# Optimization experiments

Measured on AMD Instinct MI355X. Metric: run time of the kernel, lower is better.

## Reference

```python
import jax, jax.numpy as jnp
import numpy as np

N = 50000      # nodes (atoms)
E = 1000000    # edges (bonds within cutoff)
L = 3          # num_interactions
G = 512        # graphs in batch
H = 128        # hidden_channels == num_filters
NGAUSS = 50    # num_gaussians
CUTOFF = 10.0
ZMAX = 100     # atomic numbers, < num_embeddings=120
LOG2 = float(np.log(2.0))


def ssp(x):
    # ShiftedSoftplus: softplus(x) - log(2)
    return jax.nn.softplus(x) - LOG2


def setup_inputs() -> dict:
    key = jax.random.key(0)
    ks = jax.random.split(key, 16)

    def w(k, shape, fan_in):
        return jax.random.normal(k, shape, jnp.float32) / np.sqrt(fan_in)

    z = jax.random.randint(ks[0], (N,), 1, ZMAX)
    edge_src = jax.random.randint(ks[1], (E,), 0, N)
    edge_dst = jax.random.randint(ks[2], (E,), 0, N)
    batch = jnp.sort(jax.random.randint(ks[3], (N,), 0, G))
    edge_weight = jax.random.uniform(ks[4], (E,), jnp.float32) * CUTOFF  # distances in [0, cutoff)
    edge_attr = jax.random.normal(ks[5], (E, NGAUSS), jnp.float32)       # gaussian-smeared distances
    return {
        'z': z, 'edge_src': edge_src, 'edge_dst': edge_dst, 'batch': batch,
        'num_graphs': G,
        'edge_weight': edge_weight, 'edge_attr': edge_attr,
        'emb': w(ks[6], (120, H), 1.0),
        'mlp_w1': w(ks[7], (L, NGAUSS, H), NGAUSS), 'mlp_b1': jnp.zeros((L, H), jnp.float32),
        'mlp_w2': w(ks[8], (L, H, H), H), 'mlp_b2': jnp.zeros((L, H), jnp.float32),
        'cf_w1': w(ks[9], (L, H, H), H),
        'cf_w2': w(ks[10], (L, H, H), H), 'cf_b2': jnp.zeros((L, H), jnp.float32),
        'lin_w': w(ks[11], (L, H, H), H), 'lin_b': jnp.zeros((L, H), jnp.float32),
        'ro_w1': w(ks[12], (H, 5 * H), H), 'ro_b1': jnp.zeros((5 * H,), jnp.float32),
        'ro_w2': w(ks[13], (5 * H, H), 5 * H), 'ro_b2': jnp.zeros((H,), jnp.float32),
        'ro_w3': w(ks[14], (H, 1), H), 'ro_b3': jnp.zeros((1,), jnp.float32),
    }


def reference(z, edge_src, edge_dst, batch, num_graphs, edge_weight, edge_attr,
              emb, mlp_w1, mlp_b1, mlp_w2, mlp_b2, cf_w1, cf_w2, cf_b2,
              lin_w, lin_b, ro_w1, ro_b1, ro_w2, ro_b2, ro_w3, ro_b3):
    n_nodes = z.shape[0]
    # simple_z=True: h = relu(Embedding(z))
    h = jax.nn.relu(emb[z])                                   # [N, H]
    # cosine cutoff on distances (shared across blocks)
    C = 0.5 * (jnp.cos(edge_weight * jnp.pi / CUTOFF) + 1.0)  # [E]
    for l in range(L):
        # SchNet filter network on edge attributes
        Wf = ssp(edge_attr @ mlp_w1[l] + mlp_b1[l]) @ mlp_w2[l] + mlp_b2[l]
        Wf = Wf * C[:, None]                                  # [E, H]
        x = h @ cf_w1[l]                                      # CFConv.lin1 (no bias)
        msg = x[edge_src] * Wf                                # gather + filter modulation
        agg = jax.ops.segment_sum(msg, edge_dst, num_segments=n_nodes)  # scatter-add
        x = agg @ cf_w2[l] + cf_b2[l]                         # CFConv.lin2
        x = ssp(x) @ lin_w[l] + lin_b[l]                      # act + block linear
        h = h + x                                             # residual from model forward
    # ReadOutLayer
    hh = ssp(h @ ro_w1 + ro_b1)                               # [N, 5H]
    pooled = jax.ops.segment_sum(hh, batch, num_segments=num_graphs)  # segment_csr 'add'
    out = ssp(pooled @ ro_w2 + ro_b2) @ ro_w3 + ro_b3         # [G, 1]
    return out
```

## Files before the change

kernel.cpp:

```cpp
#include <hip/hip_runtime.h>
#include <math.h>

#define N_NODES 50000
#define N_EDGES 1000000
#define LAYERS  3
#define G_GRAPHS 512
#define H 128
#define NG 50
#define PI_F 3.14159265358979323846f
#define LOG2_F 0.6931471805599453f

typedef __attribute__((ext_vector_type(4))) float f32x4;
typedef __attribute__((ext_vector_type(8))) short short8;

__device__ __forceinline__ float ssp(float v) {
    float t = __expf(-fabsf(v));
    return fmaxf(v, 0.0f) + __logf(1.0f + t) - LOG2_F;
}

__device__ __forceinline__ unsigned short f2bf(float f) {
    unsigned u = __float_as_uint(f);
    unsigned r = (u + 0x7fff + ((u >> 16) & 1)) >> 16;
    return (unsigned short)r;
}
__device__ __forceinline__ float bf2f(unsigned short h) {
    return __uint_as_float((unsigned)h << 16);
}

__global__ __launch_bounds__(256) void init_h(const int* __restrict__ z,
                                              const float* __restrict__ emb,
                                              float* __restrict__ h) {
    int idx = blockIdx.x * 256 + threadIdx.x;
    if (idx >= N_NODES * (H / 4)) return;
    int n = idx >> 5;
    int c4 = idx & 31;
    int zv = z[n];
    float4 v = *(const float4*)(emb + (size_t)zv * H + c4 * 4);
    v.x = fmaxf(v.x, 0.f); v.y = fmaxf(v.y, 0.f);
    v.z = fmaxf(v.z, 0.f); v.w = fmaxf(v.w, 0.f);
    *(float4*)(h + (size_t)n * H + c4 * 4) = v;
}

__global__ __launch_bounds__(256) void hist_kernel(const int* __restrict__ edst,
                                                   int* __restrict__ cnt) {
    int e = blockIdx.x * 256 + threadIdx.x;
    if (e < N_EDGES) atomicAdd(&cnt[edst[e]], 1);
}

__global__ __launch_bounds__(1024) void scan_kernel(const int* __restrict__ cnt,
                                                    int* __restrict__ cur) {
    __shared__ int wsum[16];
    __shared__ int carry_s;
    int tid = threadIdx.x;
    int wid = tid >> 6, lane = tid & 63;
    if (tid == 0) carry_s = 0;
    __syncthreads();
    for (int base = 0; base < N_NODES; base += 1024) {
        int i = base + tid;
        int v = (i < N_NODES) ? cnt[i] : 0;
        int s = v;
#pragma unroll
        for (int d = 1; d < 64; d <<= 1) {
            int t = __shfl_up(s, d, 64);
            if (lane >= d) s += t;
        }
        if (lane == 63) wsum[wid] = s;
        __syncthreads();
        if (wid == 0) {
            int ws = (lane < 16) ? wsum[lane] : 0;
#pragma unroll
            for (int d = 1; d < 16; d <<= 1) {
                int t = __shfl_up(ws, d, 64);
                if (lane >= d) ws += t;
            }
            if (lane < 16) wsum[lane] = ws;
        }
        __syncthreads();
        int waveoff = (wid > 0) ? wsum[wid - 1] : 0;
        int carry = carry_s;
        if (i < N_NODES) cur[i] = carry + waveoff + s - v;
        __syncthreads();
        if (tid == 1023) carry_s = carry + wsum[15];
    }
}

__global__ __launch_bounds__(256) void scatter_kernel(const int* __restrict__ edst,
                                                      int* __restrict__ cur,
                                                      int* __restrict__ perm) {
    int e = blockIdx.x * 256 + threadIdx.x;
    if (e < N_EDGES) {
        int p = atomicAdd(&cur[edst[e]], 1);
        perm[p] = e;
    }
}

__global__ __launch_bounds__(256) void conv_w(const float* __restrict__ mlp_w1,
                                              const float* __restrict__ mlp_w2,
                                              unsigned short* __restrict__ w1t,
                                              unsigned short* __restrict__ w2t) {
    int idx = blockIdx.x * 256 + threadIdx.x;
    const int n1 = LAYERS * 128 * 64;
    if (idx < n1) {
        int l = idx / (128 * 64);
        int rem = idx - l * 128 * 64;
        int col = rem >> 6, k = rem & 63;
        float v = (k < NG) ? mlp_w1[(size_t)l * NG * H + (size_t)k * H + col] : 0.f;
        w1t[idx] = f2bf(v);
        return;
    }
    int idx2 = idx - n1;
    if (idx2 < LAYERS * 128 * 128) {
        int l = idx2 / (128 * 128);
        int rem = idx2 - l * 128 * 128;
        int col = rem >> 7, k = rem & 127;
        w2t[idx2] = f2bf(mlp_w2[(size_t)l * H * H + (size_t)k * H + col]);
    }
}

__global__ __launch_bounds__(256) void conv_nodew(const float* __restrict__ src,
                                                  unsigned short* __restrict__ hi,
                                                  unsigned short* __restrict__ lo,
                                                  int ncols) {
    int idx = blockIdx.x * 256 + threadIdx.x;
    if (idx >= ncols * 128) return;
    int col = idx >> 7, k = idx & 127;
    float v = src[(size_t)k * ncols + col];
    unsigned short h16 = f2bf(v);
    hi[idx] = h16;
    lo[idx] = f2bf(v - bf2f(h16));
}

#define F_BIAS 1
#define F_POOL 8

template <int FLAGS>
__global__ __launch_bounds__(256, 4) void node_gemm_mfma(const float* __restrict__ A,
                                                         const unsigned short* __restrict__ BtHi,
                                                         const unsigned short* __restrict__ BtLo,
                                                         const float* __restrict__ bias,
                                                         float* __restrict__ Out,
                                                         const int* __restrict__ batch,
                                                         int nRows, int NC) {
    __shared__ __align__(16) char ldsHi[64 * 256];
    __shared__ __align__(16) char ldsLo[64 * 256];
    int tid = threadIdx.x;
    int rowBase = blockIdx.x * 64;
    int colOff = blockIdx.y * 128;
    int rlim = nRows - rowBase; if (rlim > 64) rlim = 64;

    for (int idx = tid; idx < 64 * 32; idx += 256) {
        int r = idx >> 5, q = idx & 31;
        float4 v = make_float4(0.f, 0.f, 0.f, 0.f);
        if (r < rlim) v = *(const float4*)(A + (size_t)(rowBase + r) * H + q * 4);
        unsigned short h0 = f2bf(v.x), h1 = f2bf(v.y), h2 = f2bf(v.z), h3 = f2bf(v.w);
        unsigned short l0 = f2bf(v.x - bf2f(h0)), l1 = f2bf(v.y - bf2f(h1));
        unsigned short l2 = f2bf(v.z - bf2f(h2)), l3 = f2bf(v.w - bf2f(h3));
        int byte = (r << 8) + (q << 3);
        byte ^= (r & 7) << 4;
        *(uint2*)(ldsHi + byte) = make_uint2((unsigned)h0 | ((unsigned)h1 << 16),
                                             (unsigned)h2 | ((unsigned)h3 << 16));
        *(uint2*)(ldsLo + byte) = make_uint2((unsigned)l0 | ((unsigned)l1 << 16),
                                             (unsigned)l2 | ((unsigned)l3 << 16));
    }
    __syncthreads();

    int w = tid >> 6, lane = tid & 63;
    int lg = lane >> 4, cg = lane & 15;
    int swA = (cg & 7) << 4;

    f32x4 acc[4][2];
#pragma unroll
    for (int n = 0; n < 2; ++n) {
        float b = (FLAGS & F_BIAS) ? bias[colOff + w * 32 + n * 16 + cg] : 0.f;
        f32x4 t = {b, b, b, b};
#pragma unroll
        for (int m = 0; m < 4; ++m) acc[m][n] = t;
    }

#pragma unroll
    for (int kc = 0; kc < 4; ++kc) {
        short8 aHi[4], aLo[4], bHi[2], bLo[2];
#pragma unroll
        for (int m = 0; m < 4; ++m) {
            int byte = ((m * 16 + cg) << 8) + ((kc * 32 + lg * 8) << 1);
            aHi[m] = *(short8*)(ldsHi + (byte ^ swA));
            aLo[m] = *(short8*)(ldsLo + (byte ^ swA));
        }
#pragma unroll
        for (int n = 0; n < 2; ++n) {
            size_t off = (size_t)(colOff + w * 32 + n * 16 + cg) * 128 + kc * 32 + lg * 8;
            bHi[n] = *(const short8*)(BtHi + off);
            bLo[n] = *(const short8*)(BtLo + off);
        }
#pragma unroll
        for (int m = 0; m < 4; ++m)
#pragma unroll
            for (int n = 0; n < 2; ++n) {
                acc[m][n] = __builtin_amdgcn_mfma_f32_16x16x32_bf16(aHi[m], bHi[n], acc[m][n], 0, 0, 0);
                acc[m][n] = __builtin_amdgcn_mfma_f32_16x16x32_bf16(aLo[m], bHi[n], acc[m][n], 0, 0, 0);
                acc[m][n] = __builtin_amdgcn_mfma_f32_16x16x32_bf16(aHi[m], bLo[n], acc[m][n], 0, 0, 0);
            }
    }

    if (FLAGS & F_POOL) {
        int cur = -1;
        float s[2] = {0.f, 0.f};
#pragma unroll
        for (int m = 0; m < 4; ++m) {
#pragma unroll
            for (int i = 0; i < 4; ++i) {
                int row = m * 16 + lg * 4 + i;
                int b = (row < rlim) ? batch[rowBase + row] : -1;
                if (b != cur) {
                    if (cur >= 0) {
#pragma unroll
                        for (int n = 0; n < 2; ++n)
                            unsafeAtomicAdd(Out + (size_t)cur * NC + colOff + w * 32 + n * 16 + cg, s[n]);
                    }
                    cur = b;
                    s[0] = 0.f; s[1] = 0.f;
                }
                if (b >= 0) {
#pragma unroll
                    for (int n = 0; n < 2; ++n) s[n] += ssp(acc[m][n][i]);
                }
            }
        }
        if (cur >= 0) {
#pragma unroll
            for (int n = 0; n < 2; ++n)
                unsafeAtomicAdd(Out + (size_t)cur * NC + colOff + w * 32 + n * 16 + cg, s[n]);
        }
    } else {
#pragma unroll
        for (int m = 0; m < 4; ++m)
#pragma unroll
            for (int i = 0; i < 4; ++i) {
                int row = m * 16 + lg * 4 + i;
                if (row < rlim) {
#pragma unroll
                    for (int n = 0; n < 2; ++n)
                        Out[(size_t)(rowBase + row) * NC + colOff + w * 32 + n * 16 + cg] = acc[m][n][i];
                }
            }
    }
}

__global__ __launch_bounds__(256, 4) void node_gemm2_mfma(const float* __restrict__ Agg,
                                                          const unsigned short* __restrict__ W2hi,
                                                          const unsigned short* __restrict__ W2lo,
                                                          const float* __restrict__ b2,
                                                          const unsigned short* __restrict__ WLhi,
                                                          const unsigned short* __restrict__ WLlo,
                                                          const float* __restrict__ bl,
                                                          float* __restrict__ Hio,
                                                          int nRows) {
    __shared__ __align__(16) char ldsHi[64 * 256];
    __shared__ __align__(16) char ldsLo[64 * 256];
    int tid = threadIdx.x;
    int rowBase = blockIdx.x * 64;
    int rlim = nRows - rowBase; if (rlim > 64) rlim = 64;

    for (int idx = tid; idx < 64 * 32; idx += 256) {
        int r = idx >> 5, q = idx & 31;
        float4 v = make_float4(0.f, 0.f, 0.f, 0.f);
        if (r < rlim) v = *(const float4*)(Agg + (size_t)(rowBase + r) * H + q * 4);
        unsigned short h0 = f2bf(v.x), h1 = f2bf(v.y), h2 = f2bf(v.z), h3 = f2bf(v.w);
        unsigned short l0 = f2bf(v.x - bf2f(h0)), l1 = f2bf(v.y - bf2f(h1));
        unsigned short l2 = f2bf(v.z - bf2f(h2)), l3 = f2bf(v.w - bf2f(h3));
        int byte = (r << 8) + (q << 3);
        byte ^= (r & 7) << 4;
        *(uint2*)(ldsHi + byte) = make_uint2((unsigned)h0 | ((unsigned)h1 << 16),
                                             (unsigned)h2 | ((unsigned)h3 << 16));
        *(uint2*)(ldsLo + byte) = make_uint2((unsigned)l0 | ((unsigned)l1 << 16),
                                             (unsigned)l2 | ((unsigned)l3 << 16));
    }
    __syncthreads();

    int w = tid >> 6, lane = tid & 63;
    int lg = lane >> 4, cg = lane & 15;
    int swA = (cg & 7) << 4;

    f32x4 acc[4][2];
#pragma unroll
    for (int n = 0; n < 2; ++n) {
        float b = b2[w * 32 + n * 16 + cg];
        f32x4 t = {b, b, b, b};
#pragma unroll
        for (int m = 0; m < 4; ++m) acc[m][n] = t;
    }
#pragma unroll
    for (int kc = 0; kc < 4; ++kc) {
        short8 aHi[4], aLo[4], bHi[2], bLo[2];
#pragma unroll
        for (int m = 0; m < 4; ++m) {
            int byte = ((m * 16 + cg) << 8) + ((kc * 32 + lg * 8) << 1);
            aHi[m] = *(short8*)(ldsHi + (byte ^ swA));
            aLo[m] = *(short8*)(ldsLo + (byte ^ swA));
        }
#pragma unroll
        for (int n = 0; n < 2; ++n) {
            size_t off = (size_t)(w * 32 + n * 16 + cg) * 128 + kc * 32 + lg * 8;
            bHi[n] = *(const short8*)(W2hi + off);
            bLo[n] = *(const short8*)(W2lo + off);
        }
#pragma unroll
        for (int m = 0; m < 4; ++m)
#pragma unroll
            for (int n = 0; n < 2; ++n) {
                acc[m][n] = __builtin_amdgcn_mfma_f32_16x16x32_bf16(aHi[m], bHi[n], acc[m][n], 0, 0, 0);
                acc[m][n] = __builtin_amdgcn_mfma_f32_16x16x32_bf16(aLo[m], bHi[n], acc[m][n], 0, 0, 0);
                acc[m][n] = __builtin_amdgcn_mfma_f32_16x16x32_bf16(aHi[m], bLo[n], acc[m][n], 0, 0, 0);
            }
    }
    __syncthreads();

#pragma unroll
    for (int m = 0; m < 4; ++m)
#pragma unroll
        for (int n = 0; n < 2; ++n)
#pragma unroll
            for (int i = 0; i < 4; ++i) {
                int row = m * 16 + lg * 4 + i;
                int col = w * 32 + n * 16 + cg;
                float v = ssp(acc[m][n][i]);
                unsigned short hh = f2bf(v);
                unsigned short ll = f2bf(v - bf2f(hh));
                int byte = (row << 8) + (col << 1);
                byte ^= (row & 7) << 4;
                *(unsigned short*)(ldsHi + byte) = hh;
                *(unsigned short*)(ldsLo + byte) = ll;
            }
    __syncthreads();

    f32x4 acc2[4][2];
#pragma unroll
    for (int n = 0; n < 2; ++n) {
        float b = bl[w * 32 + n * 16 + cg];
        f32x4 t = {b, b, b, b};
#pragma unroll
        for (int m = 0; m < 4; ++m) acc2[m][n] = t;
    }
#pragma unroll
    for (int kc = 0; kc < 4; ++kc) {
        short8 aHi[4], aLo[4], bHi[2], bLo[2];
#pragma unroll
        for (int m = 0; m < 4; ++m) {
            int byte = ((m * 16 + cg) << 8) + ((kc * 32 + lg * 8) << 1);
            aHi[m] = *(short8*)(ldsHi + (byte ^ swA));
            aLo[m] = *(short8*)(ldsLo + (byte ^ swA));
        }
#pragma unroll
        for (int n = 0; n < 2; ++n) {
            size_t off = (size_t)(w * 32 + n * 16 + cg) * 128 + kc * 32 + lg * 8;
            bHi[n] = *(const short8*)(WLhi + off);
            bLo[n] = *(const short8*)(WLlo + off);
        }
#pragma unroll
        for (int m = 0; m < 4; ++m)
#pragma unroll
            for (int n = 0; n < 2; ++n) {
                acc2[m][n] = __builtin_amdgcn_mfma_f32_16x16x32_bf16(aHi[m], bHi[n], acc2[m][n], 0, 0, 0);
                acc2[m][n] = __builtin_amdgcn_mfma_f32_16x16x32_bf16(aLo[m], bHi[n], acc2[m][n], 0, 0, 0);
                acc2[m][n] = __builtin_amdgcn_mfma_f32_16x16x32_bf16(aHi[m], bLo[n], acc2[m][n], 0, 0, 0);
            }
    }

#pragma unroll
    for (int m = 0; m < 4; ++m)
#pragma unroll
        for (int i = 0; i < 4; ++i) {
            int row = m * 16 + lg * 4 + i;
            if (row < rlim) {
#pragma unroll
                for (int n = 0; n < 2; ++n) {
                    float* p = Hio + (size_t)(rowBase + row) * H + w * 32 + n * 16 + cg;
                    *p += acc2[m][n][i];
                }
            }
        }
}

__global__ __launch_bounds__(256, 4) void edge_kernel(const float* __restrict__ eattr,
                                                      const float* __restrict__ ew,
                                                      const int* __restrict__ esrc,
                                                      const int* __restrict__ edst,
                                                      const int* __restrict__ perm,
                                                      const unsigned short* __restrict__ W1t,
                                                      const float* __restrict__ b1,
                                                      const unsigned short* __restrict__ W2t,
                                                      const float* __restrict__ b2,
                                                      const float* __restrict__ x,
                                                      float* __restrict__ agg) {
    __shared__ __align__(16) char lds_buf[64 * 132 * 4];
    __shared__ float Ce[64];
    __shared__ int Se[64], De[64], Ge[64], Rid[64], RunDst[64];
    __shared__ int s_bound[2];

    int tid = threadIdx.x;
    int e0 = blockIdx.x * 64;

    if (tid < 64) {
        int ge = perm[e0 + tid];
        Ge[tid] = ge;
        Se[tid] = esrc[ge];
        De[tid] = edst[ge];
        Ce[tid] = 0.5f * (cosf(ew[ge] * (PI_F / 10.0f)) + 1.0f);
    }
    if (tid == 64) s_bound[0] = (e0 > 0) ? edst[perm[e0 - 1]] : -1;
    if (tid == 65) s_bound[1] = (e0 + 64 < N_EDGES) ? edst[perm[e0 + 64]] : -1;
    __syncthreads();

    for (int idx = tid; idx < 64 * 32; idx += 256) {
        int e = idx >> 5, k2 = idx & 31;
        float a0 = 0.f, a1 = 0.f;
        if (k2 < 25) {
            float2 v = *(const float2*)(eattr + (size_t)Ge[e] * NG + 2 * k2);
            a0 = v.x; a1 = v.y;
        }
        unsigned p = (unsigned)f2bf(a0) | ((unsigned)f2bf(a1) << 16);
        int byte = (e << 7) + (k2 << 2);
        byte ^= (e & 7) << 4;
        *(unsigned*)(lds_buf + byte) = p;
    }
    if (tid < 64) {
        int f = (tid > 0 && De[tid] != De[tid - 1]) ? 1 : 0;
#pragma unroll
        for (int s = 1; s < 64; s <<= 1) {
            int o = __shfl_up(f, s, 64);
            if (tid >= s) f += o;
        }
        Rid[tid] = f;
        RunDst[f] = De[tid];
    }
    __syncthreads();

    int w = tid >> 6, lane = tid & 63;
    int lg = lane >> 4, cg = lane & 15;
    int eB = w * 16 + cg;
    int swz = (eB & 7) << 4;
    int le0 = w * 16 + lg * 4;

    f32x4 acc1[8];
#pragma unroll
    for (int mt = 0; mt < 8; ++mt)
        acc1[mt] = *(const f32x4*)(b1 + mt * 16 + lg * 4);
#pragma unroll
    for (int kc = 0; kc < 2; ++kc) {
        int byteB = (eB << 7) + (kc << 6) + (lg << 4);
        short8 bfrag = *(short8*)(lds_buf + (byteB ^ swz));
#pragma unroll
        for (int mt = 0; mt < 8; ++mt) {
            short8 afrag = *(const short8*)(W1t + ((mt * 16 + cg) << 6) + (kc << 5) + (lg << 3));
            acc1[mt] = __builtin_amdgcn_mfma_f32_16x16x32_bf16(afrag, bfrag, acc1[mt], 0, 0, 0);
        }
    }
#pragma unroll
    for (int mt = 0; mt < 8; ++mt) {
        f32x4 v = acc1[mt];
        unsigned p0 = (unsigned)f2bf(ssp(v[0])) | ((unsigned)f2bf(ssp(v[1])) << 16);
        unsigned p1 = (unsigned)f2bf(ssp(v[2])) | ((unsigned)f2bf(ssp(v[3])) << 16);
        int byte = 8192 + (eB << 8) + (mt << 5) + (lg << 3);
        *(uint2*)(lds_buf + (byte ^ swz)) = make_uint2(p0, p1);
    }
    __syncthreads();

    f32x4 acc2[8];
#pragma unroll
    for (int n = 0; n < 8; ++n) {
        float bb = b2[n * 16 + cg];
        f32x4 t = {bb, bb, bb, bb};
        acc2[n] = t;
    }
#pragma unroll
    for (int kc = 0; kc < 4; ++kc) {
        int byteA = 8192 + (eB << 8) + (kc << 6) + (lg << 4);
        short8 afrag = *(short8*)(lds_buf + (byteA ^ swz));
#pragma unroll
        for (int n = 0; n < 8; ++n) {
            short8 bfrag = *(const short8*)(W2t + ((n * 16 + cg) << 7) + (kc << 5) + (lg << 3));
            acc2[n] = __builtin_amdgcn_mfma_f32_16x16x32_bf16(afrag, bfrag, acc2[n], 0, 0, 0);
        }
    }

    float xv[4][8];
#pragma unroll
    for (int i = 0; i < 4; ++i) {
        const float* xrow = x + (size_t)Se[le0 + i] * H + cg;
#pragma unroll
        for (int n = 0; n < 8; ++n) xv[i][n] = xrow[n * 16];
    }
    asm volatile("s_waitcnt lgkmcnt(0)" ::: "memory");
    __builtin_amdgcn_s_barrier();

    float* accT = (float*)lds_buf;
    int nruns = Rid[63] + 1;
    for (int idx = tid; idx < nruns * 132; idx += 256) accT[idx] = 0.f;
    __syncthreads();

    int curR = -1;
    float part[8];
#pragma unroll
    for (int i = 0; i < 4; ++i) {
        int le = le0 + i;
        int r = Rid[le];
        float cf = Ce[le];
        float m[8];
#pragma unroll
        for (int n = 0; n < 8; ++n) m[n] = xv[i][n] * acc2[n][i] * cf;
        if (r != curR) {
            if (curR >= 0) {
#pragma unroll
                for (int n = 0; n < 8; ++n)
                    atomicAdd(accT + curR * 132 + n * 16 + cg, part[n]);
            }
            curR = r;
#pragma unroll
            for (int n = 0; n < 8; ++n) part[n] = m[n];
        } else {
#pragma unroll
            for (int n = 0; n < 8; ++n) part[n] += m[n];
        }
    }
#pragma unroll
    for (int n = 0; n < 8; ++n)
        atomicAdd(accT + curR * 132 + n * 16 + cg, part[n]);
    __syncthreads();

    int prevd = s_bound[0], nextd = s_bound[1];
    for (int idx = tid; idx < nruns * H; idx += 256) {
        int r = idx >> 7, c = idx & 127;
        float v = accT[r * 132 + c];
        int d = RunDst[r];
        bool shared_run = (r == 0 && d == prevd) || (r == nruns - 1 && d == nextd);
        float* p = agg + (size_t)d * H + c;
        if (shared_run) unsafeAtomicAdd(p, v);
        else *p = v;
    }
}

__global__ __launch_bounds__(128) void final_out(const float* __restrict__ pooled,
                                                 const float* __restrict__ ro_w2,
                                                 const float* __restrict__ ro_b2,
                                                 const float* __restrict__ ro_w3,
                                                 const float* __restrict__ ro_b3,
                                                 float* __restrict__ out) {
    int g = blockIdx.x;
    int c = threadIdx.x;
    float acc = ro_b2[c];
    const float* pr = pooled + (size_t)g * (5 * H);
    for (int k = 0; k < 5 * H; ++k) acc = fmaf(pr[k], ro_w2[(size_t)k * H + c], acc);
    float v = ssp(acc) * ro_w3[c];
    __shared__ float red[128];
    red[c] = v;
    __syncthreads();
    for (int s = 64; s > 0; s >>= 1) {
        if (c < s) red[c] += red[c + s];
        __syncthreads();
    }
    if (c == 0) out[g] = red[0] + ro_b3[0];
}

extern "C" void kernel_launch(void* const* d_in, const int* in_sizes, int n_in,
                              void* d_out, int out_size, void* d_ws, size_t ws_size,
                              hipStream_t stream) {
    const int* z     = (const int*)d_in[0];
    const int* esrc  = (const int*)d_in[1];
    const int* edst  = (const int*)d_in[2];
    const int* batch = (const int*)d_in[3];
    const float* ew    = (const float*)d_in[5];
    const float* eattr = (const float*)d_in[6];
    const float* emb   = (const float*)d_in[7];
    const float* mlp_w1 = (const float*)d_in[8];
    const float* mlp_b1 = (const float*)d_in[9];
    const float* mlp_w2 = (const float*)d_in[10];
    const float* mlp_b2 = (const float*)d_in[11];
    const float* cf_w1  = (const float*)d_in[12];
    const float* cf_w2  = (const float*)d_in[13];
    const float* cf_b2  = (const float*)d_in[14];
    const float* lin_w  = (const float*)d_in[15];
    const float* lin_b  = (const float*)d_in[16];
    const float* ro_w1  = (const float*)d_in[17];
    const float* ro_b1  = (const float*)d_in[18];
    const float* ro_w2  = (const float*)d_in[19];
    const float* ro_b2  = (const float*)d_in[20];
    const float* ro_w3  = (const float*)d_in[21];
    const float* ro_b3  = (const float*)d_in[22];
    float* out = (float*)d_out;

    float* h      = (float*)d_ws;
    float* x      = h + (size_t)N_NODES * H;
    float* agg    = x + (size_t)N_NODES * H;
    float* pooled = agg + (size_t)N_NODES * H;
    int*   cnt    = (int*)(pooled + (size_t)G_GRAPHS * 5 * H);
    int*   cur    = cnt + N_NODES;
    int*   perm   = cur + N_NODES;
    unsigned short* w1t  = (unsigned short*)(perm + N_EDGES);
    unsigned short* w2t  = w1t + (size_t)LAYERS * 128 * 64;
    unsigned short* nwhi = w2t + (size_t)LAYERS * 128 * 128;
    unsigned short* nwlo = nwhi + (size_t)(9 * 16384 + 640 * 128);

    init_h<<<(N_NODES * (H / 4) + 255) / 256, 256, 0, stream>>>(z, emb, h);

    conv_w<<<(LAYERS * 128 * 64 + LAYERS * 128 * 128 + 255) / 256, 256, 0, stream>>>(
        mlp_w1, mlp_w2, w1t, w2t);
    for (int l = 0; l < LAYERS; ++l) {
        conv_nodew<<<(128 * 128 + 255) / 256, 256, 0, stream>>>(
            cf_w1 + (size_t)l * H * H, nwhi + (size_t)l * 16384, nwlo + (size_t)l * 16384, 128);
        conv_nodew<<<(128 * 128 + 255) / 256, 256, 0, stream>>>(
            cf_w2 + (size_t)l * H * H, nwhi + (size_t)(3 + l) * 16384, nwlo + (size_t)(3 + l) * 16384, 128);
        conv_nodew<<<(128 * 128 + 255) / 256, 256, 0, stream>>>(
            lin_w + (size_t)l * H * H, nwhi + (size_t)(6 + l) * 16384, nwlo + (size_t)(6 + l) * 16384, 128);
    }
    conv_nodew<<<(640 * 128 + 255) / 256, 256, 0, stream>>>(
        ro_w1, nwhi + (size_t)9 * 16384, nwlo + (size_t)9 * 16384, 640);

    hipMemsetAsync(cnt, 0, N_NODES * sizeof(int), stream);
    hist_kernel<<<(N_EDGES + 255) / 256, 256, 0, stream>>>(edst, cnt);
    scan_kernel<<<1, 1024, 0, stream>>>(cnt, cur);
    scatter_kernel<<<(N_EDGES + 255) / 256, 256, 0, stream>>>(edst, cur, perm);

    int rowTiles = (N_NODES + 63) / 64;
    for (int l = 0; l < LAYERS; ++l) {
        node_gemm_mfma<0><<<dim3(rowTiles, 1), 256, 0, stream>>>(
            h, nwhi + (size_t)l * 16384, nwlo + (size_t)l * 16384, nullptr, x, nullptr, N_NODES, H);
        hipMemsetAsync(agg, 0, (size_t)N_NODES * H * sizeof(float), stream);
        edge_kernel<<<N_EDGES / 64, 256, 0, stream>>>(
            eattr, ew, esrc, edst, perm,
            w1t + (size_t)l * 128 * 64, mlp_b1 + (size_t)l * H,
            w2t + (size_t)l * 128 * 128, mlp_b2 + (size_t)l * H, x, agg);
        node_gemm2_mfma<<<dim3(rowTiles, 1), 256, 0, stream>>>(
            agg,
            nwhi + (size_t)(3 + l) * 16384, nwlo + (size_t)(3 + l) * 16384, cf_b2 + (size_t)l * H,
            nwhi + (size_t)(6 + l) * 16384, nwlo + (size_t)(6 + l) * 16384, lin_b + (size_t)l * H,
            h, N_NODES);
    }

    hipMemsetAsync(pooled, 0, (size_t)G_GRAPHS * 5 * H * sizeof(float), stream);
    node_gemm_mfma<F_BIAS | F_POOL><<<dim3(rowTiles, 5), 256, 0, stream>>>(
        h, nwhi + (size_t)9 * 16384, nwlo + (size_t)9 * 16384, ro_b1, pooled, batch, N_NODES, 5 * H);
    final_out<<<G_GRAPHS, 128, 0, stream>>>(pooled, ro_w2, ro_b2, ro_w3, ro_b3, out);
}
```

Before: 2.308 ms.

## Pre-permute edge indices and bf16 attributes once, slim edge kernel LDS and syncs

Adds one-time prep kernels that store src, dst and cutoff coefficients, plus bf16-packed edge attributes, in dst-sorted order. The three per-layer edge kernels then read contiguous data instead of gathering through perm three times. The edge kernel also computes run ids in registers with wave shuffles, caps LDS accumulation at 8 runs (spilling extra runs straight to global atomics), removes several block barriers and shrinks LDS to allow 5 blocks per CU. In exchange it uses about 140MB more workspace and adds a fallback path for when the workspace is too small.

```diff
diff --git a/kernel.cpp b/kernel.cpp
--- a/kernel.cpp
+++ b/kernel.cpp
@@ -92,6 +92,49 @@
         int p = atomicAdd(&cur[edst[e]], 1);
         perm[p] = e;
     }
+}
+
+__global__ __launch_bounds__(256) void prep_idx(const int* __restrict__ perm,
+                                                const int* __restrict__ esrc,
+                                                const int* __restrict__ edst,
+                                                const float* __restrict__ ew,
+                                                int* __restrict__ Sp,
+                                                int* __restrict__ Dp,
+                                                float* __restrict__ Cp) {
+    int pos = blockIdx.x * 256 + threadIdx.x;
+    if (pos >= N_EDGES) return;
+    int ge = perm[pos];
+    Sp[pos] = esrc[ge];
+    Dp[pos] = edst[ge];
+    Cp[pos] = 0.5f * (cosf(ew[ge] * (PI_F / 10.0f)) + 1.0f);
+}
+
+__global__ __launch_bounds__(256) void prep_attr(const int* __restrict__ perm,
+                                                 const float* __restrict__ eattr,
+                                                 unsigned short* __restrict__ pattr) {
+    int t = blockIdx.x * 256 + threadIdx.x;
+    int pos = t >> 3, kq = t & 7;
+    if (pos >= N_EDGES) return;
+    int ge = perm[pos];
+    int k0 = kq * 8;
+    float v[8] = {0.f, 0.f, 0.f, 0.f, 0.f, 0.f, 0.f, 0.f};
+    const float* row = eattr + (size_t)ge * NG;
+    if (k0 + 8 <= NG) {
+#pragma unroll
+        for (int q = 0; q < 4; ++q) {
+            float2 a = *(const float2*)(row + k0 + 2 * q);
+            v[2 * q] = a.x; v[2 * q + 1] = a.y;
+        }
+    } else if (k0 < NG) {
+        float2 a = *(const float2*)(row + k0);
+        v[0] = a.x; v[1] = a.y;
+    }
+    uint4 wv;
+    wv.x = (unsigned)f2bf(v[0]) | ((unsigned)f2bf(v[1]) << 16);
+    wv.y = (unsigned)f2bf(v[2]) | ((unsigned)f2bf(v[3]) << 16);
+    wv.z = (unsigned)f2bf(v[4]) | ((unsigned)f2bf(v[5]) << 16);
+    wv.w = (unsigned)f2bf(v[6]) | ((unsigned)f2bf(v[7]) << 16);
+    *(uint4*)(pattr + (size_t)pos * 64 + k0) = wv;
 }
 
 __global__ __launch_bounds__(256) void conv_w(const float* __restrict__ mlp_w1,
@@ -381,61 +424,76 @@
         }
 }
 
-__global__ __launch_bounds__(256, 4) void edge_kernel(const float* __restrict__ eattr,
-                                                      const float* __restrict__ ew,
-                                                      const int* __restrict__ esrc,
-                                                      const int* __restrict__ edst,
-                                                      const int* __restrict__ perm,
-                                                      const unsigned short* __restrict__ W1t,
-                                                      const float* __restrict__ b1,
-                                                      const unsigned short* __restrict__ W2t,
-                                                      const float* __restrict__ b2,
-                                                      const float* __restrict__ x,
-                                                      float* __restrict__ agg) {
-    __shared__ __align__(16) char lds_buf[64 * 132 * 4];
-    __shared__ float Ce[64];
-    __shared__ int Se[64], De[64], Ge[64], Rid[64], RunDst[64];
-    __shared__ int s_bound[2];
+template <bool IDXP, bool ATTRP>
+__global__ __launch_bounds__(256, 5) void edge_kernel(
+        const unsigned short* __restrict__ pattr,
+        const float* __restrict__ eattr,
+        const int* __restrict__ perm,
+        const int* __restrict__ esrc,
+        const int* __restrict__ edst,
+        const float* __restrict__ ew,
+        const int* __restrict__ Sp,
+        const int* __restrict__ Dp,
+        const float* __restrict__ Cp,
+        const unsigned short* __restrict__ W1t,
+        const float* __restrict__ b1,
+        const unsigned short* __restrict__ W2t,
+        const float* __restrict__ b2,
+        const float* __restrict__ x,
+        float* __restrict__ agg) {
+    __shared__ __align__(16) char lds[28832];
+    float* accT = (float*)(lds + 24576);
+    int* RunDst = (int*)(lds + 28800);
 
     int tid = threadIdx.x;
     int e0 = blockIdx.x * 64;
-
-    if (tid < 64) {
-        int ge = perm[e0 + tid];
-        Ge[tid] = ge;
-        Se[tid] = esrc[ge];
-        De[tid] = edst[ge];
-        Ce[tid] = 0.5f * (cosf(ew[ge] * (PI_F / 10.0f)) + 1.0f);
-    }
-    if (tid == 64) s_bound[0] = (e0 > 0) ? edst[perm[e0 - 1]] : -1;
-    if (tid == 65) s_bound[1] = (e0 + 64 < N_EDGES) ? edst[perm[e0 + 64]] : -1;
-    __syncthreads();
-
-    for (int idx = tid; idx < 64 * 32; idx += 256) {
-        int e = idx >> 5, k2 = idx & 31;
-        float a0 = 0.f, a1 = 0.f;
-        if (k2 < 25) {
-            float2 v = *(const float2*)(eattr + (size_t)Ge[e] * NG + 2 * k2);
-            a0 = v.x; a1 = v.y;
-        }
-        unsigned p = (unsigned)f2bf(a0) | ((unsigned)f2bf(a1) << 16);
-        int byte = (e << 7) + (k2 << 2);
-        byte ^= (e & 7) << 4;
-        *(unsigned*)(lds_buf + byte) = p;
-    }
-    if (tid < 64) {
-        int f = (tid > 0 && De[tid] != De[tid - 1]) ? 1 : 0;
-#pragma unroll
-        for (int s = 1; s < 64; s <<= 1) {
-            int o = __shfl_up(f, s, 64);
-            if (tid >= s) f += o;
-        }
-        Rid[tid] = f;
-        RunDst[f] = De[tid];
-    }
-    __syncthreads();
-
     int w = tid >> 6, lane = tid & 63;
+
+    for (int i = tid; i < 8 * 132; i += 256) accT[i] = 0.f;
+
+    int ge = 0;
+    if (!ATTRP || !IDXP) ge = perm[e0 + lane];
+    int S, D; float C;
+    if (IDXP) {
+        S = Sp[e0 + lane]; D = Dp[e0 + lane]; C = Cp[e0 + lane];
+    } else {
+        S = esrc[ge]; D = edst[ge];
+        C = 0.5f * (cosf(ew[ge] * (PI_F / 10.0f)) + 1.0f);
+    }
+    int prevd = -1, nextd = -1;
+    if (e0 > 0)            prevd = IDXP ? Dp[e0 - 1]  : edst[perm[e0 - 1]];
+    if (e0 + 64 < N_EDGES) nextd = IDXP ? Dp[e0 + 64] : edst[perm[e0 + 64]];
+
+    if (ATTRP) {
+#pragma unroll
+        for (int half = 0; half < 2; ++half) {
+            int idx2 = lane + half * 64;
+            int row = w * 16 + (idx2 >> 3);
+            int q = idx2 & 7;
+            uint4 v = *(const uint4*)(pattr + (((size_t)(e0 + row)) << 6) + q * 8);
+            int byte = (row << 7) + (q << 4);
+            byte ^= (row & 7) << 4;
+            *(uint4*)(lds + byte) = v;
+        }
+    } else {
+        int row = w * 16 + (lane >> 2);
+        int grow = __shfl(ge, row);
+        int jbase = (lane & 3) * 8;
+#pragma unroll
+        for (int j = 0; j < 8; ++j) {
+            int k2 = jbase + j;
+            float a0 = 0.f, a1 = 0.f;
+            if (k2 < 25) {
+                float2 t = *(const float2*)(eattr + (size_t)grow * NG + 2 * k2);
+                a0 = t.x; a1 = t.y;
+            }
+            unsigned p = (unsigned)f2bf(a0) | ((unsigned)f2bf(a1) << 16);
+            int byte = (row << 7) + (k2 << 2);
+            byte ^= (row & 7) << 4;
+            *(unsigned*)(lds + byte) = p;
+        }
+    }
+
     int lg = lane >> 4, cg = lane & 15;
     int eB = w * 16 + cg;
     int swz = (eB & 7) << 4;
@@ -448,7 +506,7 @@
 #pragma unroll
     for (int kc = 0; kc < 2; ++kc) {
         int byteB = (eB << 7) + (kc << 6) + (lg << 4);
-        short8 bfrag = *(short8*)(lds_buf + (byteB ^ swz));
+        short8 bfrag = *(short8*)(lds + (byteB ^ swz));
 #pragma unroll
         for (int mt = 0; mt < 8; ++mt) {
             short8 afrag = *(const short8*)(W1t + ((mt * 16 + cg) << 6) + (kc << 5) + (lg << 3));
@@ -461,9 +519,8 @@
         unsigned p0 = (unsigned)f2bf(ssp(v[0])) | ((unsigned)f2bf(ssp(v[1])) << 16);
         unsigned p1 = (unsigned)f2bf(ssp(v[2])) | ((unsigned)f2bf(ssp(v[3])) << 16);
         int byte = 8192 + (eB << 8) + (mt << 5) + (lg << 3);
-        *(uint2*)(lds_buf + (byte ^ swz)) = make_uint2(p0, p1);
-    }
-    __syncthreads();
+        *(uint2*)(lds + (byte ^ swz)) = make_uint2(p0, p1);
+    }
 
     f32x4 acc2[8];
 #pragma unroll
@@ -475,7 +532,7 @@
 #pragma unroll
     for (int kc = 0; kc < 4; ++kc) {
         int byteA = 8192 + (eB << 8) + (kc << 6) + (lg << 4);
-        short8 afrag = *(short8*)(lds_buf + (byteA ^ swz));
+        short8 afrag = *(short8*)(lds + (byteA ^ swz));
 #pragma unroll
         for (int n = 0; n < 8; ++n) {
             short8 bfrag = *(const short8*)(W2t + ((n * 16 + cg) << 7) + (kc << 5) + (lg << 3));
@@ -486,35 +543,51 @@
     float xv[4][8];
 #pragma unroll
     for (int i = 0; i < 4; ++i) {
-        const float* xrow = x + (size_t)Se[le0 + i] * H + cg;
+        int sle = __shfl(S, le0 + i);
+        const float* xrow = x + (size_t)sle * H + cg;
 #pragma unroll
         for (int n = 0; n < 8; ++n) xv[i][n] = xrow[n * 16];
     }
+
+    int dprev = __shfl_up(D, 1, 64);
+    int flag = (lane > 0 && D != dprev) ? 1 : 0;
+    int rid = flag;
+#pragma unroll
+    for (int s2 = 1; s2 < 64; s2 <<= 1) {
+        int o = __shfl_up(rid, s2, 64);
+        if (lane >= s2) rid += o;
+    }
+    int nruns = __shfl(rid, 63) + 1;
+    if (w == 0 && (lane == 0 || flag) && rid < 8) RunDst[rid] = D;
+
     asm volatile("s_waitcnt lgkmcnt(0)" ::: "memory");
     __builtin_amdgcn_s_barrier();
-
-    float* accT = (float*)lds_buf;
-    int nruns = Rid[63] + 1;
-    for (int idx = tid; idx < nruns * 132; idx += 256) accT[idx] = 0.f;
-    __syncthreads();
-
-    int curR = -1;
+    asm volatile("" ::: "memory");
+
+    int curR = -1, curD = 0;
     float part[8];
 #pragma unroll
     for (int i = 0; i < 4; ++i) {
         int le = le0 + i;
-        int r = Rid[le];
-        float cf = Ce[le];
+        int r  = __shfl(rid, le);
+        int dd = __shfl(D, le);
+        float cf = __shfl(C, le);
         float m[8];
 #pragma unroll
         for (int n = 0; n < 8; ++n) m[n] = xv[i][n] * acc2[n][i] * cf;
         if (r != curR) {
             if (curR >= 0) {
-#pragma unroll
-                for (int n = 0; n < 8; ++n)
-                    atomicAdd(accT + curR * 132 + n * 16 + cg, part[n]);
-            }
-            curR = r;
+                if (curR < 8) {
+#pragma unroll
+                    for (int n = 0; n < 8; ++n)
+                        atomicAdd(accT + curR * 132 + n * 16 + cg, part[n]);
+                } else {
+#pragma unroll
+                    for (int n = 0; n < 8; ++n)
+                        unsafeAtomicAdd(agg + (size_t)curD * H + n * 16 + cg, part[n]);
+                }
+            }
+            curR = r; curD = dd;
 #pragma unroll
             for (int n = 0; n < 8; ++n) part[n] = m[n];
         } else {
@@ -522,13 +595,22 @@
             for (int n = 0; n < 8; ++n) part[n] += m[n];
         }
     }
-#pragma unroll
-    for (int n = 0; n < 8; ++n)
-        atomicAdd(accT + curR * 132 + n * 16 + cg, part[n]);
-    __syncthreads();
-
-    int prevd = s_bound[0], nextd = s_bound[1];
-    for (int idx = tid; idx < nruns * H; idx += 256) {
+    if (curR < 8) {
+#pragma unroll
+        for (int n = 0; n < 8; ++n)
+            atomicAdd(accT + curR * 132 + n * 16 + cg, part[n]);
+    } else {
+#pragma unroll
+        for (int n = 0; n < 8; ++n)
+            unsafeAtomicAdd(agg + (size_t)curD * H + n * 16 + cg, part[n]);
+    }
+
+    asm volatile("s_waitcnt lgkmcnt(0)" ::: "memory");
+    __builtin_amdgcn_s_barrier();
+    asm volatile("" ::: "memory");
+
+    int nstore = (nruns < 8) ? nruns : 8;
+    for (int idx = tid; idx < nstore * H; idx += 256) {
         int r = idx >> 7, c = idx & 127;
         float v = accT[r * 132 + c];
         int d = RunDst[r];
@@ -588,17 +670,32 @@
     const float* ro_b3  = (const float*)d_in[22];
     float* out = (float*)d_out;
 
-    float* h      = (float*)d_ws;
-    float* x      = h + (size_t)N_NODES * H;
-    float* agg    = x + (size_t)N_NODES * H;
-    float* pooled = agg + (size_t)N_NODES * H;
-    int*   cnt    = (int*)(pooled + (size_t)G_GRAPHS * 5 * H);
-    int*   cur    = cnt + N_NODES;
-    int*   perm   = cur + N_NODES;
-    unsigned short* w1t  = (unsigned short*)(perm + N_EDGES);
-    unsigned short* w2t  = w1t + (size_t)LAYERS * 128 * 64;
-    unsigned short* nwhi = w2t + (size_t)LAYERS * 128 * 128;
-    unsigned short* nwlo = nwhi + (size_t)(9 * 16384 + 640 * 128);
+    char* wp = (char*)d_ws;
+    auto alloc = [&](size_t bytes) {
+        char* p = wp;
+        wp += (bytes + 255) & ~(size_t)255;
+        return p;
+    };
+    float* h      = (float*)alloc((size_t)N_NODES * H * 4);
+    float* x      = (float*)alloc((size_t)N_NODES * H * 4);
+    float* agg    = (float*)alloc((size_t)N_NODES * H * 4);
+    float* pooled = (float*)alloc((size_t)G_GRAPHS * 5 * H * 4);
+    int*   cnt    = (int*)alloc(N_NODES * 4);
+    int*   cur    = (int*)alloc(N_NODES * 4);
+    int*   perm   = (int*)alloc((size_t)N_EDGES * 4);
+    unsigned short* w1t  = (unsigned short*)alloc((size_t)LAYERS * 128 * 64 * 2);
+    unsigned short* w2t  = (unsigned short*)alloc((size_t)LAYERS * 128 * 128 * 2);
+    unsigned short* nwhi = (unsigned short*)alloc((size_t)(9 * 16384 + 640 * 128) * 2);
+    unsigned short* nwlo = (unsigned short*)alloc((size_t)(9 * 16384 + 640 * 128) * 2);
+    int*   Sp = (int*)alloc((size_t)N_EDGES * 4);
+    int*   Dp = (int*)alloc((size_t)N_EDGES * 4);
+    float* Cp = (float*)alloc((size_t)N_EDGES * 4);
+    size_t used_idx = (size_t)(wp - (char*)d_ws);
+    unsigned short* pattr = (unsigned short*)alloc((size_t)N_EDGES * 64 * 2);
+    size_t used_attr = (size_t)(wp - (char*)d_ws);
+
+    bool idxp  = ws_size >= used_idx;
+    bool attrp = ws_size >= used_attr;
 
     init_h<<<(N_NODES * (H / 4) + 255) / 256, 256, 0, stream>>>(z, emb, h);
 
@@ -620,15 +717,31 @@
     scan_kernel<<<1, 1024, 0, stream>>>(cnt, cur);
     scatter_kernel<<<(N_EDGES + 255) / 256, 256, 0, stream>>>(edst, cur, perm);
 
+    if (idxp)
+        prep_idx<<<(N_EDGES + 255) / 256, 256, 0, stream>>>(perm, esrc, edst, ew, Sp, Dp, Cp);
+    if (attrp)
+        prep_attr<<<(N_EDGES * 8 + 255) / 256, 256, 0, stream>>>(perm, eattr, pattr);
+
     int rowTiles = (N_NODES + 63) / 64;
     for (int l = 0; l < LAYERS; ++l) {
         node_gemm_mfma<0><<<dim3(rowTiles, 1), 256, 0, stream>>>(
             h, nwhi + (size_t)l * 16384, nwlo + (size_t)l * 16384, nullptr, x, nullptr, N_NODES, H);
         hipMemsetAsync(agg, 0, (size_t)N_NODES * H * sizeof(float), stream);
-        edge_kernel<<<N_EDGES / 64, 256, 0, stream>>>(
-            eattr, ew, esrc, edst, perm,
-            w1t + (size_t)l * 128 * 64, mlp_b1 + (size_t)l * H,
-            w2t + (size_t)l * 128 * 128, mlp_b2 + (size_t)l * H, x, agg);
+        if (attrp)
+            edge_kernel<true, true><<<N_EDGES / 64, 256, 0, stream>>>(
+                pattr, eattr, perm, esrc, edst, ew, Sp, Dp, Cp,
+                w1t + (size_t)l * 128 * 64, mlp_b1 + (size_t)l * H,
+                w2t + (size_t)l * 128 * 128, mlp_b2 + (size_t)l * H, x, agg);
+        else if (idxp)
+            edge_kernel<true, false><<<N_EDGES / 64, 256, 0, stream>>>(
+                pattr, eattr, perm, esrc, edst, ew, Sp, Dp, Cp,
+                w1t + (size_t)l * 128 * 64, mlp_b1 + (size_t)l * H,
+                w2t + (size_t)l * 128 * 128, mlp_b2 + (size_t)l * H, x, agg);
+        else
+            edge_kernel<false, false><<<N_EDGES / 64, 256, 0, stream>>>(
+                pattr, eattr, perm, esrc, edst, ew, Sp, Dp, Cp,
+                w1t + (size_t)l * 128 * 64, mlp_b1 + (size_t)l * H,
+                w2t + (size_t)l * 128 * 128, mlp_b2 + (size_t)l * H, x, agg);
         node_gemm2_mfma<<<dim3(rowTiles, 1), 256, 0, stream>>>(
             agg,
             nwhi + (size_t)(3 + l) * 16384, nwlo + (size_t)(3 + l) * 16384, cf_b2 + (size_t)l * H,
```

Result: faster. 2.027 ms (-12.2%).
